# Kernel tuning notes

Measured on AMD Instinct MI355X. Metric: run time of the kernel, lower is better.

## Reference

```python
import jax, jax.numpy as jnp
import numpy as np
from jax import lax

NUM_HEADS = 8
DIM = 192
EPS = 1e-12  # torch F.normalize eps


def setup_inputs() -> dict:
    key = jax.random.key(0)
    k1, k2, k3, k4 = jax.random.split(key, 4)
    b, c, h, w = 8, DIM, 128, 128
    x = jax.random.normal(k1, (b, c, h, w), dtype=jnp.float32)
    # 1x1 qkv conv weight stored as [3c, c]; depthwise 3x3 weight [3c,1,3,3]; proj 1x1 [c,c]
    w_qkv = jax.random.normal(k2, (3 * c, c), dtype=jnp.float32) * (1.0 / np.sqrt(c))
    w_dw = jax.random.normal(k3, (3 * c, 1, 3, 3), dtype=jnp.float32) * (1.0 / 3.0)
    w_proj = jax.random.normal(k4, (c, c), dtype=jnp.float32) * (1.0 / np.sqrt(c))
    temperature = jnp.ones((NUM_HEADS, 1, 1), dtype=jnp.float32)
    return {"x": x, "w_qkv": w_qkv, "w_dw": w_dw, "w_proj": w_proj, "temperature": temperature}


def _l2_normalize(t):
    # matches torch.nn.functional.normalize(dim=-1, eps=1e-12)
    n = jnp.sqrt(jnp.sum(t * t, axis=-1, keepdims=True))
    return t / jnp.maximum(n, EPS)


def reference(x, w_qkv, w_dw, w_proj, temperature):
    b, c, h, w = x.shape
    heads = NUM_HEADS
    cd = c // heads  # per-head channel dim
    # 1x1 qkv conv (no bias) as einsum
    qkv = jnp.einsum('bchw,oc->bohw', x, w_qkv)  # [b, 3c, h, w]
    # depthwise 3x3 conv, groups = 3c
    qkv = lax.conv_general_dilated(
        qkv, w_dw, window_strides=(1, 1), padding='SAME',
        feature_group_count=3 * c,
        dimension_numbers=('NCHW', 'OIHW', 'NCHW'))
    q, k, v = jnp.split(qkv, 3, axis=1)  # each [b, c, h, w]
    hw = h * w
    q = q.reshape(b, heads, cd, hw)
    k = k.reshape(b, heads, cd, hw)
    v = v.reshape(b, heads, cd, hw)
    q = _l2_normalize(q)
    k = _l2_normalize(k)
    # channel-wise attention: [b, heads, cd, cd]
    attn = jnp.einsum('bhcn,bhdn->bhcd', q, k) * temperature[None]
    attn = jax.nn.softmax(attn, axis=-1)
    out = jnp.einsum('bhcd,bhdn->bhcn', attn, v)  # [b, heads, cd, hw]
    out = out.reshape(b, c, h, w)
    out = jnp.einsum('bchw,oc->bohw', out, w_proj)
    return out
```

## Files before the change

kernel.cpp:

```cpp
#include <hip/hip_runtime.h>

#define HW 16384
#define CC 192
#define C3 576
#define NB 8
#define NH 8

typedef __attribute__((ext_vector_type(8))) short bfrag;
typedef __attribute__((ext_vector_type(4))) float f32x4;
typedef __attribute__((ext_vector_type(4))) unsigned short us4;

#define MFMA16(a, b, c) __builtin_amdgcn_mfma_f32_16x16x32_bf16(a, b, c, 0, 0, 0)

typedef __attribute__((address_space(3))) unsigned int lds_u32;
typedef __attribute__((address_space(1))) unsigned int glb_u32;
__device__ __forceinline__ void gl_lds16(const void* g, void* l) {
  __builtin_amdgcn_global_load_lds((const glb_u32*)g, (lds_u32*)l, 16, 0, 0);
}

__device__ __forceinline__ unsigned short f2bf(float f) {
  unsigned int u = __float_as_uint(f);
  u += 0x7fffu + ((u >> 16) & 1u);
  return (unsigned short)(u >> 16);
}
__device__ __forceinline__ float bf2f(unsigned short s) {
  return __uint_as_float(((unsigned int)s) << 16);
}
__device__ __forceinline__ float bf2f_s(short s) {
  return __uint_as_float(((unsigned int)(unsigned short)s) << 16);
}

#define OFF_XT   0ull
#define SZ_XT    ((size_t)NB * HW * CC * 2)
#define OFF_WQ   (OFF_XT + SZ_XT)
#define SZ_WQ    ((size_t)C3 * CC * 2)
#define OFF_QKV  (OFF_WQ + SZ_WQ)
#define SZ_QKV   ((size_t)NB * C3 * HW * 2)
#define OFF_S    (OFF_QKV + SZ_QKV)
#define SZ_S     ((size_t)NB * NH * 32 * 32 * 4)
#define OFF_SSQ  (OFF_S + SZ_S)
#define SZ_SSQ   ((size_t)NB * 384 * 4)
#define OFF_M    (OFF_SSQ + SZ_SSQ)
#define SZ_M     ((size_t)NB * CC * CC * 2)

__global__ __launch_bounds__(256) void k_xt(const float* __restrict__ x,
                                            unsigned short* __restrict__ xt) {
  __shared__ unsigned short tile[64 * 72];
  const int pb = blockIdx.x * 64;
  const int cb = blockIdx.y * 64;
  const int b  = blockIdx.z;
  const int t  = threadIdx.x;
  {
    const int cl = t >> 2, pl = (t & 3) * 16;
    const float* src = x + ((size_t)b * CC + cb + cl) * HW + pb + pl;
    bfrag v0, v1;
#pragma unroll
    for (int q4 = 0; q4 < 2; ++q4) {
      float4 f = *reinterpret_cast<const float4*>(src + q4 * 4);
      v0[q4 * 4 + 0] = (short)f2bf(f.x); v0[q4 * 4 + 1] = (short)f2bf(f.y);
      v0[q4 * 4 + 2] = (short)f2bf(f.z); v0[q4 * 4 + 3] = (short)f2bf(f.w);
    }
#pragma unroll
    for (int q4 = 0; q4 < 2; ++q4) {
      float4 f = *reinterpret_cast<const float4*>(src + 8 + q4 * 4);
      v1[q4 * 4 + 0] = (short)f2bf(f.x); v1[q4 * 4 + 1] = (short)f2bf(f.y);
      v1[q4 * 4 + 2] = (short)f2bf(f.z); v1[q4 * 4 + 3] = (short)f2bf(f.w);
    }
    *reinterpret_cast<bfrag*>(&tile[cl * 72 + pl]) = v0;
    *reinterpret_cast<bfrag*>(&tile[cl * 72 + pl + 8]) = v1;
  }
  __syncthreads();
  {
    const int pl = t >> 2, cl = (t & 3) * 16;
    bfrag o0, o1;
#pragma unroll
    for (int e = 0; e < 8; ++e) o0[e] = (short)tile[(cl + e) * 72 + pl];
#pragma unroll
    for (int e = 0; e < 8; ++e) o1[e] = (short)tile[(cl + 8 + e) * 72 + pl];
    unsigned short* dst = xt + ((size_t)b * HW + pb + pl) * CC + cb + cl;
    *reinterpret_cast<bfrag*>(dst) = o0;
    *reinterpret_cast<bfrag*>(dst + 8) = o1;
  }
}

__global__ __launch_bounds__(256) void k_wpack(const float* __restrict__ w,
                                               unsigned short* __restrict__ wp) {
  const int g = blockIdx.x * 256 + threadIdx.x;
  if (g >= 216 * 64) return;
  const int frag = g >> 6, lane = g & 63;
  const int mb = frag / 24, r = frag % 24, s = r >> 2, i = r & 3;
  const int row = mb * 64 + i * 16 + (lane & 15);
  const int col = s * 32 + (lane >> 4) * 8;
  const float* src = w + (size_t)row * CC + col;
  float4 f0 = *reinterpret_cast<const float4*>(src);
  float4 f1 = *reinterpret_cast<const float4*>(src + 4);
  us4 o0, o1;
  o0[0] = f2bf(f0.x); o0[1] = f2bf(f0.y); o0[2] = f2bf(f0.z); o0[3] = f2bf(f0.w);
  o1[0] = f2bf(f1.x); o1[1] = f2bf(f1.y); o1[2] = f2bf(f1.z); o1[3] = f2bf(f1.w);
  *reinterpret_cast<us4*>(wp + (size_t)g * 8) = o0;
  *reinterpret_cast<us4*>(wp + (size_t)g * 8 + 4) = o1;
}

__global__ __launch_bounds__(256, 3) void k_gemm_qkv(const unsigned short* __restrict__ Wp,
                                                     const unsigned short* __restrict__ Xt,
                                                     unsigned short* __restrict__ Y) {
  __shared__ __attribute__((aligned(16))) char sB[49152];
  const int nb = blockIdx.x;
  const int b  = blockIdx.y;
  const int tid = threadIdx.x;
  const int wave = tid >> 6, lane = tid & 63;
  const int lrow = lane & 15, lk = (lane >> 4) * 8, lr4 = (lane >> 4) * 4;

  const char* Bc = (const char*)(Xt + ((size_t)b * HW + (size_t)nb * 128) * CC);
#pragma unroll
  for (int t = 0; t < 12; ++t) {
    const int L = wave * 12288 + t * 1024 + lane * 16;
    const int row = L / 384;
    const int rem = L - row * 384;
    gl_lds16(Bc + row * 384 + (rem ^ ((row & 7) << 4)), sB + wave * 12288 + t * 1024);
  }
  asm volatile("s_waitcnt vmcnt(0)" ::: "memory");
  __syncthreads();

  const int swz = (lrow & 7) << 4;
  const int base0 = (wave * 32 + lrow) * 384;
  const f32x4 z4 = {0.f, 0.f, 0.f, 0.f};

#pragma unroll 1
  for (int mb = 0; mb < 9; ++mb) {
    const unsigned short* Wb = Wp + (size_t)mb * 24 * 512;
    bfrag af[6][4];
#pragma unroll
    for (int s = 0; s < 6; ++s)
#pragma unroll
      for (int i = 0; i < 4; ++i)
        af[s][i] = *reinterpret_cast<const bfrag*>(Wb + ((s * 4 + i) * 64 + lane) * 8);

    f32x4 acc[4][2];
#pragma unroll
    for (int i = 0; i < 4; ++i) { acc[i][0] = z4; acc[i][1] = z4; }
#pragma unroll
    for (int s = 0; s < 6; ++s) {
      const int kbs = ((s * 32 + lk) * 2) ^ swz;
      bfrag b0 = *reinterpret_cast<const bfrag*>(sB + base0 + kbs);
      bfrag b1 = *reinterpret_cast<const bfrag*>(sB + base0 + 16 * 384 + kbs);
#pragma unroll
      for (int i = 0; i < 4; ++i) {
        acc[i][0] = MFMA16(b0, af[s][i], acc[i][0]);
        acc[i][1] = MFMA16(b1, af[s][i], acc[i][1]);
      }
    }
    unsigned short* Yb = Y + ((size_t)b * C3 + mb * 64) * HW + nb * 128 + wave * 32;
#pragma unroll
    for (int i = 0; i < 4; ++i) {
      unsigned short* rp = Yb + (size_t)(i * 16 + lrow) * HW;
#pragma unroll
      for (int j = 0; j < 2; ++j) {
        uint2 pk;
        pk.x = (unsigned int)f2bf(acc[i][j][0]) | ((unsigned int)f2bf(acc[i][j][1]) << 16);
        pk.y = (unsigned int)f2bf(acc[i][j][2]) | ((unsigned int)f2bf(acc[i][j][3]) << 16);
        *reinterpret_cast<uint2*>(rp + j * 16 + lr4) = pk;
      }
    }
  }
}

__global__ __launch_bounds__(256, 2) void k_dwgram(const unsigned short* __restrict__ QKV,
                                                   const float* __restrict__ wd,
                                                   float* __restrict__ S,
                                                   float* __restrict__ ssq) {
  __shared__ short lds[56 * 520];
  const int strip = blockIdx.x, h = blockIdx.y, b = blockIdx.z;
  const int tid = threadIdx.x, wave = tid >> 6, lane = tid & 63;
  const int lrow = lane & 15, lk8 = (lane >> 4) * 8, lr4 = (lane >> 4) * 4;
  const size_t qbase = ((size_t)b * C3 + h * 24) * HW;
  const size_t kbase = qbase + (size_t)192 * HW;

  const int p = lane * 8;
  const int x0 = p & 127;

  float sqp[6] = {0.f, 0.f, 0.f, 0.f, 0.f, 0.f};
  float skp[6] = {0.f, 0.f, 0.f, 0.f, 0.f, 0.f};
  f32x4 acc[2][2];
  const f32x4 z4 = {0.f, 0.f, 0.f, 0.f};
#pragma unroll
  for (int i = 0; i < 2; ++i) { acc[i][0] = z4; acc[i][1] = z4; }

  auto dwconv8 = [&](const unsigned short* ip, const float* w, int y, float* facc) {
#pragma unroll
    for (int e = 0; e < 8; ++e) facc[e] = 0.f;
#pragma unroll
    for (int dy = 0; dy < 3; ++dy) {
      int yy = y + dy - 1;
      if (yy < 0 || yy > 127) continue;
      const unsigned short* row = ip + yy * 128;
      bfrag v = *reinterpret_cast<const bfrag*>(row + x0);
      float c[8];
#pragma unroll
      for (int e = 0; e < 8; ++e) c[e] = bf2f_s(v[e]);
      float left  = (x0 > 0)   ? bf2f(row[x0 - 1]) : 0.f;
      float right = (x0 < 120) ? bf2f(row[x0 + 8]) : 0.f;
      float wl = w[dy * 3 + 0], wc = w[dy * 3 + 1], wr = w[dy * 3 + 2];
      facc[0] += wl * left + wc * c[0] + wr * c[1];
#pragma unroll
      for (int e = 1; e < 7; ++e) facc[e] += wl * c[e - 1] + wc * c[e] + wr * c[e + 1];
      facc[7] += wl * c[6] + wc * c[7] + wr * right;
    }
  };

#pragma unroll 1
  for (int chunk = 0; chunk < 4; ++chunk) {
    const int y = strip * 16 + chunk * 4 + (p >> 7);
#pragma unroll
    for (int j = 0; j < 6; ++j) {
      const int c = wave + 4 * j;
      float faccq[8], facck[8];
      dwconv8(QKV + qbase + (size_t)c * HW, wd + (h * 24 + c) * 9, y, faccq);
      dwconv8(QKV + kbase + (size_t)c * HW, wd + (192 + h * 24 + c) * 9, y, facck);
      {
        float ss = 0.f;
        bfrag o;
#pragma unroll
        for (int e = 0; e < 8; ++e) { ss += faccq[e] * faccq[e]; o[e] = (short)f2bf(faccq[e]); }
        sqp[j] += ss;
        *reinterpret_cast<bfrag*>(&lds[c * 520 + p]) = o;
      }
      {
        float ss = 0.f;
        bfrag o;
#pragma unroll
        for (int e = 0; e < 8; ++e) { ss += facck[e] * facck[e]; o[e] = (short)f2bf(facck[e]); }
        skp[j] += ss;
        *reinterpret_cast<bfrag*>(&lds[(24 + c) * 520 + p]) = o;
      }
    }
    __syncthreads();
#pragma unroll
    for (int ks = 0; ks < 4; ++ks) {
      const int pp = wave * 128 + ks * 32 + lk8;
      bfrag aq[2], bk[2];
#pragma unroll
      for (int i = 0; i < 2; ++i) {
        aq[i] = *reinterpret_cast<const bfrag*>(&lds[(i * 16 + lrow) * 520 + pp]);
        bk[i] = *reinterpret_cast<const bfrag*>(&lds[(24 + i * 16 + lrow) * 520 + pp]);
      }
#pragma unroll
      for (int i = 0; i < 2; ++i)
#pragma unroll
        for (int j2 = 0; j2 < 2; ++j2) acc[i][j2] = MFMA16(aq[i], bk[j2], acc[i][j2]);
    }
    __syncthreads();
  }

  float* Sb = S + (size_t)(b * 8 + h) * 1024;
#pragma unroll
  for (int i = 0; i < 2; ++i)
#pragma unroll
    for (int j2 = 0; j2 < 2; ++j2)
#pragma unroll
      for (int r = 0; r < 4; ++r)
        atomicAdd(&Sb[(i * 16 + lr4 + r) * 32 + j2 * 16 + lrow], acc[i][j2][r]);

#pragma unroll
  for (int j = 0; j < 6; ++j) {
    float v = sqp[j];
    float wv = skp[j];
#pragma unroll
    for (int o = 1; o < 64; o <<= 1) { v += __shfl_xor(v, o); wv += __shfl_xor(wv, o); }
    if (lane == 0) {
      const int c = wave + 4 * j;
      atomicAdd(&ssq[b * 384 + h * 24 + c], v);
      atomicAdd(&ssq[b * 384 + 192 + h * 24 + c], wv);
    }
  }
}

__global__ __launch_bounds__(256) void k_dwvt(const unsigned short* __restrict__ QKV,
                                              const float* __restrict__ wd,
                                              unsigned short* __restrict__ VTo) {
  __shared__ unsigned short tile[64 * 72];
  const int pb = blockIdx.x * 64, cb = blockIdx.y * 64, b = blockIdx.z;
  const int t = threadIdx.x;
  const int y = pb >> 7;
  const int xs = pb & 127;
  {
    const int cl = t >> 2, ps = (t & 3) * 16;
    const int gc = 384 + cb + cl;
    const unsigned short* ip = QKV + ((size_t)b * C3 + gc) * HW;
    const float* w = wd + gc * 9;
    const int x0 = xs + ps;
    float acc[16];
#pragma unroll
    for (int e = 0; e < 16; ++e) acc[e] = 0.f;
#pragma unroll
    for (int dy = 0; dy < 3; ++dy) {
      int yy = y + dy - 1;
      if (yy < 0 || yy > 127) continue;
      const unsigned short* row = ip + yy * 128;
      bfrag v0 = *reinterpret_cast<const bfrag*>(row + x0);
      bfrag v1 = *reinterpret_cast<const bfrag*>(row + x0 + 8);
      float c[16];
#pragma unroll
      for (int e = 0; e < 8; ++e) { c[e] = bf2f_s(v0[e]); c[8 + e] = bf2f_s(v1[e]); }
      float left  = (x0 > 0)   ? bf2f(row[x0 - 1])  : 0.f;
      float right = (x0 < 112) ? bf2f(row[x0 + 16]) : 0.f;
      float wl = w[dy * 3 + 0], wc = w[dy * 3 + 1], wr = w[dy * 3 + 2];
      acc[0] += wl * left + wc * c[0] + wr * c[1];
#pragma unroll
      for (int e = 1; e < 15; ++e) acc[e] += wl * c[e - 1] + wc * c[e] + wr * c[e + 1];
      acc[15] += wl * c[14] + wc * c[15] + wr * right;
    }
    bfrag o0, o1;
#pragma unroll
    for (int e = 0; e < 8; ++e) { o0[e] = (short)f2bf(acc[e]); o1[e] = (short)f2bf(acc[8 + e]); }
    *reinterpret_cast<bfrag*>(&tile[cl * 72 + ps]) = o0;
    *reinterpret_cast<bfrag*>(&tile[cl * 72 + ps + 8]) = o1;
  }
  __syncthreads();
  {
    const int pl = t >> 2, cs = (t & 3) * 16;
    bfrag o0, o1;
#pragma unroll
    for (int e = 0; e < 8; ++e) o0[e] = (short)tile[(cs + e) * 72 + pl];
#pragma unroll
    for (int e = 0; e < 8; ++e) o1[e] = (short)tile[(cs + 8 + e) * 72 + pl];
    unsigned short* dst = VTo + ((size_t)b * HW + pb + pl) * CC + cb + cs;
    *reinterpret_cast<bfrag*>(dst) = o0;
    *reinterpret_cast<bfrag*>(dst + 8) = o1;
  }
}

__global__ __launch_bounds__(64) void k_attn(const float* __restrict__ S,
                                             const float* __restrict__ ssq,
                                             const float* __restrict__ wproj,
                                             const float* __restrict__ temp,
                                             unsigned short* __restrict__ Mp) {
  const int h = blockIdx.x, b = blockIdx.y;
  __shared__ float A[24][25];
  __shared__ float nq[24], nk[24];
  const float* Sb = S + (size_t)(b * 8 + h) * 1024;
  const float* sq = ssq + b * 384 + h * 24;
  const float* sk = ssq + b * 384 + 192 + h * 24;
  const int t = threadIdx.x;
  if (t < 24) {
    nq[t] = fmaxf(sqrtf(sq[t]), 1e-12f);
    nk[t] = fmaxf(sqrtf(sk[t]), 1e-12f);
  }
  __syncthreads();
  if (t < 24) {
    const float tp = temp[h];
    float row[24];
    float mx = -1e30f;
#pragma unroll
    for (int d = 0; d < 24; ++d) {
      row[d] = Sb[t * 32 + d] / (nq[t] * nk[d]) * tp;
      mx = fmaxf(mx, row[d]);
    }
    float s = 0.f;
#pragma unroll
    for (int d = 0; d < 24; ++d) { row[d] = __expf(row[d] - mx); s += row[d]; }
    const float inv = 1.f / s;
#pragma unroll
    for (int d = 0; d < 24; ++d) A[t][d] = row[d] * inv;
  }
  __syncthreads();
  for (int idx = t; idx < 192 * 24; idx += 64) {
    const int o = idx / 24, dd = idx % 24;
    const float* wrow = wproj + o * 192 + h * 24;
    float a = 0.f;
#pragma unroll
    for (int cc = 0; cc < 24; ++cc) a += wrow[cc] * A[cc][dd];
    const int c = h * 24 + dd;
    const int mb = o >> 6, i = (o >> 4) & 3, lr = o & 15;
    const int s = c >> 5, hi = (c >> 3) & 3, e = c & 7;
    const int off = ((mb * 24 + s * 4 + i) * 64 + hi * 16 + lr) * 8 + e;
    Mp[(size_t)b * CC * CC + off] = f2bf(a);
  }
}

__global__ __launch_bounds__(256, 3) void k_gemm_out(const unsigned short* __restrict__ Mp,
                                                     const unsigned short* __restrict__ VT,
                                                     float* __restrict__ out) {
  __shared__ __attribute__((aligned(16))) char sB[49152];
  const int nb = blockIdx.x;
  const int b  = blockIdx.y;
  const int tid = threadIdx.x;
  const int wave = tid >> 6, lane = tid & 63;
  const int lrow = lane & 15, lk = (lane >> 4) * 8, lr4 = (lane >> 4) * 4;

  const char* Bc = (const char*)(VT + ((size_t)b * HW + (size_t)nb * 128) * CC);
#pragma unroll
  for (int t = 0; t < 12; ++t) {
    const int L = wave * 12288 + t * 1024 + lane * 16;
    const int row = L / 384;
    const int rem = L - row * 384;
    gl_lds16(Bc + row * 384 + (rem ^ ((row & 7) << 4)), sB + wave * 12288 + t * 1024);
  }
  asm volatile("s_waitcnt vmcnt(0)" ::: "memory");
  __syncthreads();

  const int swz = (lrow & 7) << 4;
  const int base0 = (wave * 32 + lrow) * 384;
  const f32x4 z4 = {0.f, 0.f, 0.f, 0.f};

#pragma unroll 1
  for (int mb = 0; mb < 3; ++mb) {
    const unsigned short* Mb = Mp + (size_t)b * CC * CC + (size_t)mb * 24 * 512;
    bfrag af[6][4];
#pragma unroll
    for (int s = 0; s < 6; ++s)
#pragma unroll
      for (int i = 0; i < 4; ++i)
        af[s][i] = *reinterpret_cast<const bfrag*>(Mb + ((s * 4 + i) * 64 + lane) * 8);

    f32x4 acc[4][2];
#pragma unroll
    for (int i = 0; i < 4; ++i) { acc[i][0] = z4; acc[i][1] = z4; }
#pragma unroll
    for (int s = 0; s < 6; ++s) {
      const int kbs = ((s * 32 + lk) * 2) ^ swz;
      bfrag b0 = *reinterpret_cast<const bfrag*>(sB + base0 + kbs);
      bfrag b1 = *reinterpret_cast<const bfrag*>(sB + base0 + 16 * 384 + kbs);
#pragma unroll
      for (int i = 0; i < 4; ++i) {
        acc[i][0] = MFMA16(b0, af[s][i], acc[i][0]);
        acc[i][1] = MFMA16(b1, af[s][i], acc[i][1]);
      }
    }
    float* Ob = out + ((size_t)b * CC + mb * 64) * HW + nb * 128 + wave * 32;
#pragma unroll
    for (int i = 0; i < 4; ++i) {
      float* rp = Ob + (size_t)(i * 16 + lrow) * HW;
#pragma unroll
      for (int j = 0; j < 2; ++j)
        *reinterpret_cast<f32x4*>(rp + j * 16 + lr4) = acc[i][j];
    }
  }
}

extern "C" void kernel_launch(void* const* d_in, const int* in_sizes, int n_in,
                              void* d_out, int out_size, void* d_ws, size_t ws_size,
                              hipStream_t stream) {
  const float* x      = (const float*)d_in[0];
  const float* w_qkv  = (const float*)d_in[1];
  const float* w_dw   = (const float*)d_in[2];
  const float* w_proj = (const float*)d_in[3];
  const float* temp   = (const float*)d_in[4];
  float* out = (float*)d_out;
  char* ws = (char*)d_ws;

  unsigned short* XT   = (unsigned short*)(ws + OFF_XT);
  unsigned short* VT   = (unsigned short*)(ws + OFF_XT);
  unsigned short* WP   = (unsigned short*)(ws + OFF_WQ);
  unsigned short* QKV  = (unsigned short*)(ws + OFF_QKV);
  float* S   = (float*)(ws + OFF_S);
  float* SSQ = (float*)(ws + OFF_SSQ);
  unsigned short* MP  = (unsigned short*)(ws + OFF_M);

  hipMemsetAsync(ws + OFF_S, 0, SZ_S + SZ_SSQ, stream);
  k_wpack<<<54, 256, 0, stream>>>(w_qkv, WP);
  k_xt<<<dim3(HW / 64, CC / 64, NB), 256, 0, stream>>>(x, XT);
  k_gemm_qkv<<<dim3(HW / 128, NB), 256, 0, stream>>>(WP, XT, QKV);
  k_dwgram<<<dim3(8, NH, NB), 256, 0, stream>>>(QKV, w_dw, S, SSQ);
  k_dwvt<<<dim3(HW / 64, 3, NB), 256, 0, stream>>>(QKV, w_dw, VT);
  k_attn<<<dim3(NH, NB), 64, 0, stream>>>(S, SSQ, w_proj, temp, MP);
  k_gemm_out<<<dim3(HW / 128, NB), 256, 0, stream>>>(MP, VT, out);
}
```

Baseline: 343.9 us.

## Split dwgram into more blocks with 4-pixel lanes and shuffle halos

The depthwise-conv plus Gram kernel now processes 4 pixels per lane instead of 8, so each block covers 4 rows instead of 16, and the grid grows from 8 to 32 strips per head. The horizontal halo values come from lane shuffles instead of extra scalar global loads, and the LDS tile shrinks so launch bounds allow 5 blocks per CU. The aim is better occupancy and latency hiding on a grid that was only 512 blocks, at the cost of four times as many atomic adds into S and SSQ and more redundant vertical halo reads.

```diff
diff --git a/kernel.cpp b/kernel.cpp
--- a/kernel.cpp
+++ b/kernel.cpp
@@ -165,19 +165,20 @@
   }
 }
 
-__global__ __launch_bounds__(256, 2) void k_dwgram(const unsigned short* __restrict__ QKV,
+__global__ __launch_bounds__(256, 5) void k_dwgram(const unsigned short* __restrict__ QKV,
                                                    const float* __restrict__ wd,
                                                    float* __restrict__ S,
                                                    float* __restrict__ ssq) {
-  __shared__ short lds[56 * 520];
+  __shared__ short lds[56 * 264];
   const int strip = blockIdx.x, h = blockIdx.y, b = blockIdx.z;
   const int tid = threadIdx.x, wave = tid >> 6, lane = tid & 63;
   const int lrow = lane & 15, lk8 = (lane >> 4) * 8, lr4 = (lane >> 4) * 4;
   const size_t qbase = ((size_t)b * C3 + h * 24) * HW;
   const size_t kbase = qbase + (size_t)192 * HW;
 
-  const int p = lane * 8;
+  const int p = lane * 4;
   const int x0 = p & 127;
+  const int rowc = p >> 7;
 
   float sqp[6] = {0.f, 0.f, 0.f, 0.f, 0.f, 0.f};
   float skp[6] = {0.f, 0.f, 0.f, 0.f, 0.f, 0.f};
@@ -186,63 +187,65 @@
 #pragma unroll
   for (int i = 0; i < 2; ++i) { acc[i][0] = z4; acc[i][1] = z4; }
 
-  auto dwconv8 = [&](const unsigned short* ip, const float* w, int y, float* facc) {
-#pragma unroll
-    for (int e = 0; e < 8; ++e) facc[e] = 0.f;
+  auto dwconv4 = [&](const unsigned short* ip, const float* w, int y, float* facc) {
+#pragma unroll
+    for (int e = 0; e < 4; ++e) facc[e] = 0.f;
 #pragma unroll
     for (int dy = 0; dy < 3; ++dy) {
       int yy = y + dy - 1;
       if (yy < 0 || yy > 127) continue;
       const unsigned short* row = ip + yy * 128;
-      bfrag v = *reinterpret_cast<const bfrag*>(row + x0);
-      float c[8];
-#pragma unroll
-      for (int e = 0; e < 8; ++e) c[e] = bf2f_s(v[e]);
-      float left  = (x0 > 0)   ? bf2f(row[x0 - 1]) : 0.f;
-      float right = (x0 < 120) ? bf2f(row[x0 + 8]) : 0.f;
+      us4 v = *reinterpret_cast<const us4*>(row + x0);
+      float c[4];
+#pragma unroll
+      for (int e = 0; e < 4; ++e) c[e] = bf2f(v[e]);
+      float left = __shfl_up(c[3], 1);
+      left = (x0 == 0) ? 0.f : left;
+      float right = __shfl_down(c[0], 1);
+      right = (x0 == 124) ? 0.f : right;
       float wl = w[dy * 3 + 0], wc = w[dy * 3 + 1], wr = w[dy * 3 + 2];
       facc[0] += wl * left + wc * c[0] + wr * c[1];
-#pragma unroll
-      for (int e = 1; e < 7; ++e) facc[e] += wl * c[e - 1] + wc * c[e] + wr * c[e + 1];
-      facc[7] += wl * c[6] + wc * c[7] + wr * right;
+      facc[1] += wl * c[0] + wc * c[1] + wr * c[2];
+      facc[2] += wl * c[1] + wc * c[2] + wr * c[3];
+      facc[3] += wl * c[2] + wc * c[3] + wr * right;
     }
   };
 
 #pragma unroll 1
-  for (int chunk = 0; chunk < 4; ++chunk) {
-    const int y = strip * 16 + chunk * 4 + (p >> 7);
-#pragma unroll
+  for (int chunk = 0; chunk < 2; ++chunk) {
+    const int y = strip * 4 + chunk * 2 + rowc;
+#pragma unroll 2
     for (int j = 0; j < 6; ++j) {
       const int c = wave + 4 * j;
-      float faccq[8], facck[8];
-      dwconv8(QKV + qbase + (size_t)c * HW, wd + (h * 24 + c) * 9, y, faccq);
-      dwconv8(QKV + kbase + (size_t)c * HW, wd + (192 + h * 24 + c) * 9, y, facck);
+      float fq[4], fk[4];
+      dwconv4(QKV + qbase + (size_t)c * HW, wd + (h * 24 + c) * 9, y, fq);
+      dwconv4(QKV + kbase + (size_t)c * HW, wd + (192 + h * 24 + c) * 9, y, fk);
       {
+        us4 o;
         float ss = 0.f;
-        bfrag o;
-#pragma unroll
-        for (int e = 0; e < 8; ++e) { ss += faccq[e] * faccq[e]; o[e] = (short)f2bf(faccq[e]); }
+#pragma unroll
+        for (int e = 0; e < 4; ++e) { ss += fq[e] * fq[e]; o[e] = f2bf(fq[e]); }
         sqp[j] += ss;
-        *reinterpret_cast<bfrag*>(&lds[c * 520 + p]) = o;
+        *reinterpret_cast<us4*>(&lds[c * 264 + p]) = o;
       }
       {
+        us4 o;
         float ss = 0.f;
-        bfrag o;
-#pragma unroll
-        for (int e = 0; e < 8; ++e) { ss += facck[e] * facck[e]; o[e] = (short)f2bf(facck[e]); }
+#pragma unroll
+        for (int e = 0; e < 4; ++e) { ss += fk[e] * fk[e]; o[e] = f2bf(fk[e]); }
         skp[j] += ss;
-        *reinterpret_cast<bfrag*>(&lds[(24 + c) * 520 + p]) = o;
+        *reinterpret_cast<us4*>(&lds[(24 + c) * 264 + p]) = o;
       }
     }
     __syncthreads();
 #pragma unroll
-    for (int ks = 0; ks < 4; ++ks) {
-      const int pp = wave * 128 + ks * 32 + lk8;
+    for (int ks = 0; ks < 2; ++ks) {
+      const int pp = wave * 64 + ks * 32 + lk8;
       bfrag aq[2], bk[2];
 #pragma unroll
       for (int i = 0; i < 2; ++i) {
-        aq[i] = *reinterpret_cast<const bfrag*>(&lds[(i * 16 + lrow) * 520 + pp]);
-        bk[i] = *reinterpret_cast<const bfrag*>(&lds[(24 + i * 16 + lrow) * 520 + pp]);
+        aq[i] = *reinterpret_cast<const bfrag*>(&lds[(i * 16 + lrow) * 264 + pp]);
+        bk[i] = *reinterpret_cast<const bfrag*>(&lds[(24 + i * 16 + lrow) * 264 + pp]);
       }
 #pragma unroll
       for (int i = 0; i < 2; ++i)
@@ -461,7 +464,7 @@
   k_wpack<<<54, 256, 0, stream>>>(w_qkv, WP);
   k_xt<<<dim3(HW / 64, CC / 64, NB), 256, 0, stream>>>(x, XT);
   k_gemm_qkv<<<dim3(HW / 128, NB), 256, 0, stream>>>(WP, XT, QKV);
-  k_dwgram<<<dim3(8, NH, NB), 256, 0, stream>>>(QKV, w_dw, S, SSQ);
+  k_dwgram<<<dim3(32, NH, NB), 256, 0, stream>>>(QKV, w_dw, S, SSQ);
   k_dwvt<<<dim3(HW / 64, 3, NB), 256, 0, stream>>>(QKV, w_dw, VT);
   k_attn<<<dim3(NH, NB), 64, 0, stream>>>(S, SSQ, w_proj, temp, MP);
   k_gemm_out<<<dim3(HW / 128, NB), 256, 0, stream>>>(MP, VT, out);
```

Result: slower. 353.5 us (+2.8%).
